# Optimization experiments

Hardware: AMD Instinct MI355X
Metric: run time of the kernel (lower is better)

The kernel has to match this reference:

```python
import jax, jax.numpy as jnp
import numpy as np

B, C, Ci, H, W = 8, 256, 128, 64, 64
EPS = 1e-5


def conv1x1(x, w, b):
    # x: [B,C,H,W], w: [O,C], b: [O] -> [B,O,H,W]
    return jnp.einsum('bchw,oc->bohw', x, w) + b[None, :, None, None]


def maxpool2(x):
    b, c, h, w = x.shape
    return x.reshape(b, c, h // 2, 2, w // 2, 2).max(axis=(3, 5))


def setup_inputs() -> dict:
    key = jax.random.key(0)
    ks = jax.random.split(key, 12)
    s_in = 1.0 / np.sqrt(C)
    s_ic = 1.0 / np.sqrt(Ci)
    return {
        'x': jax.random.normal(ks[0], (B, C, H, W), dtype=jnp.float32),
        'g_w': jax.random.normal(ks[1], (Ci, C), dtype=jnp.float32) * s_in,
        'g_b': jax.random.normal(ks[2], (Ci,), dtype=jnp.float32) * 0.01,
        'theta_w': jax.random.normal(ks[3], (Ci, C), dtype=jnp.float32) * s_in,
        'theta_b': jax.random.normal(ks[4], (Ci,), dtype=jnp.float32) * 0.01,
        'phi_w': jax.random.normal(ks[5], (Ci, C), dtype=jnp.float32) * s_in,
        'phi_b': jax.random.normal(ks[6], (Ci,), dtype=jnp.float32) * 0.01,
        'W_w': jax.random.normal(ks[7], (C, Ci), dtype=jnp.float32) * s_ic,
        'W_b': jax.random.normal(ks[8], (C,), dtype=jnp.float32) * 0.01,
        'bn_gamma': jax.random.normal(ks[9], (C,), dtype=jnp.float32) * 0.1 + 1.0,
        'bn_beta': jax.random.normal(ks[10], (C,), dtype=jnp.float32) * 0.1,
        'bn_mean': jnp.zeros((C,), dtype=jnp.float32),
        'bn_var': jax.random.uniform(ks[11], (C,), dtype=jnp.float32) * 0.5 + 0.75,
    }


def reference(x, g_w, g_b, theta_w, theta_b, phi_w, phi_b, W_w, W_b, bn_gamma, bn_beta, bn_mean, bn_var):
    b = x.shape[0]
    # g and phi: 1x1 conv then 2x2 max-pool (sub_sample=True)
    g_x = maxpool2(conv1x1(x, g_w, g_b)).reshape(b, Ci, -1)          # [B,Ci,Np]
    g_x = jnp.transpose(g_x, (0, 2, 1))                               # [B,Np,Ci]
    theta_x = conv1x1(x, theta_w, theta_b).reshape(b, Ci, -1)         # [B,Ci,N]
    theta_x = jnp.transpose(theta_x, (0, 2, 1))                       # [B,N,Ci]
    phi_x = maxpool2(conv1x1(x, phi_w, phi_b)).reshape(b, Ci, -1)     # [B,Ci,Np]
    f = jnp.einsum('bnc,bcm->bnm', theta_x, phi_x)                    # [B,N,Np]
    f_div_C = jax.nn.softmax(f, axis=-1)                              # embedded_gaussian: plain softmax, no scaling
    y = jnp.einsum('bnm,bmc->bnc', f_div_C, g_x)                      # [B,N,Ci]
    y = jnp.transpose(y, (0, 2, 1)).reshape(b, Ci, H, W)              # [B,Ci,H,W]
    # W: 1x1 conv + BatchNorm (inference form with running stats)
    W_y = conv1x1(y, W_w, W_b)
    inv = bn_gamma / jnp.sqrt(bn_var + EPS)
    W_y = (W_y - bn_mean[None, :, None, None]) * inv[None, :, None, None] + bn_beta[None, :, None, None]
    return W_y + x
```

## Files before the change

### kernel.cpp

```cpp
#include <hip/hip_runtime.h>
#include <math.h>

#define Bn   8
#define Cc   256
#define Cin  128
#define Hh   64
#define Ww   64
#define Nn   4096
#define Npl  1024
#define EPSf 1e-5f

typedef __attribute__((ext_vector_type(8))) short    short8;
typedef __attribute__((ext_vector_type(8))) _Float16 half8;
typedef __attribute__((ext_vector_type(4))) float    floatx4;

__device__ __forceinline__ unsigned short f2bf(float f) {
    unsigned int u = __float_as_uint(f);
    u += 0x7fffu + ((u >> 16) & 1u);
    return (unsigned short)(u >> 16);
}
__device__ __forceinline__ unsigned short f2h(float f) {
    _Float16 h = (_Float16)f;
    return __builtin_bit_cast(unsigned short, h);
}
__device__ __forceinline__ float h2f(unsigned short u) {
    return (float)__builtin_bit_cast(_Float16, u);
}

__device__ __forceinline__ unsigned int cvtpk_bf16(float lo, float hi) {
    unsigned int r;
    asm("v_cvt_pk_bf16_f32 %0, %1, %2" : "=v"(r) : "v"(lo), "v"(hi));
    return r;
}

__device__ __forceinline__ void gload_lds16(const unsigned short* g, unsigned short* l) {
    __builtin_amdgcn_global_load_lds(
        (const __attribute__((address_space(1))) unsigned int*)g,
        (__attribute__((address_space(3))) unsigned int*)l, 16, 0, 0);
}

__global__ __launch_bounds__(256) void k_prep(
    const float* __restrict__ g_w, const float* __restrict__ th_w,
    const float* __restrict__ ph_w,
    const float* __restrict__ W_w, const float* __restrict__ W_b,
    const float* __restrict__ gamma, const float* __restrict__ beta,
    const float* __restrict__ mean,  const float* __restrict__ var,
    unsigned short* __restrict__ gWh,
    unsigned short* __restrict__ thWh, unsigned short* __restrict__ thWl,
    unsigned short* __restrict__ phWh, unsigned short* __restrict__ phWl,
    unsigned short* __restrict__ Wh, float* __restrict__ cvec)
{
    int i = blockIdx.x * 256 + threadIdx.x;
    if (i < 98304) {
        int seg = i >> 15;
        int idx = i & 32767;
        float v = (seg == 0 ? g_w : (seg == 1 ? th_w : ph_w))[idx];
        unsigned short hi = f2h(v);
        if (seg == 0) gWh[idx] = hi;
        else {
            (seg == 1 ? thWh : phWh)[idx] = hi;
            (seg == 1 ? thWl : phWl)[idx] = f2h(v - h2f(hi));
        }
    } else {
        int j = i - 98304;
        int o = j >> 7;
        float inv = gamma[o] * rsqrtf(var[o] + EPSf);
        Wh[j] = f2h(W_w[j] * inv);
        if (j < Cc) {
            float invi = gamma[j] * rsqrtf(var[j] + EPSf);
            cvec[j] = (W_b[j] - mean[j]) * invi + beta[j];
        }
    }
}

#define XPAD 264

__global__ __launch_bounds__(256, 2) void k_conv3(
    const float* __restrict__ x,
    const unsigned short* __restrict__ gWh,
    const unsigned short* __restrict__ thWh, const unsigned short* __restrict__ thWl,
    const unsigned short* __restrict__ phWh, const unsigned short* __restrict__ phWl,
    const float* __restrict__ g_b, const float* __restrict__ th_b,
    const float* __restrict__ ph_b,
    unsigned short* __restrict__ thetaT,
    unsigned short* __restrict__ gPc,
    unsigned short* __restrict__ phiPt)
{
    __shared__ __align__(16) unsigned short Xhi[64 * XPAD];
    __shared__ __align__(16) unsigned short Xlo[64 * XPAD];

    const int t    = threadIdx.x;
    const int w    = t >> 6;
    const int l    = t & 63;
    const int quad = l >> 4;
    const int l16  = l & 15;
    const int b    = blockIdx.x >> 6;
    const int tile = blockIdx.x & 63;
    const int ty   = tile >> 1;
    const int tx   = tile & 1;

    {
        const float4* xg = (const float4*)x;
        unsigned int* XhiW = (unsigned int*)Xhi;
        unsigned int* XloW = (unsigned int*)Xlo;
        #pragma unroll
        for (int it = 0; it < 8; ++it) {
            int idx = t + 256 * it;
            int c2  = idx >> 4;
            int p4  = idx & 15;
            int n   = (2 * ty + (p4 >> 3)) * Ww + tx * 32 + (p4 & 7) * 4;
            float4 va = xg[((size_t)(b * Cc + 2 * c2) * Nn + n) >> 2];
            float4 vb = xg[((size_t)(b * Cc + 2 * c2 + 1) * Nn + n) >> 2];
            const float fa[4] = {va.x, va.y, va.z, va.w};
            const float fb[4] = {vb.x, vb.y, vb.z, vb.w};
            #pragma unroll
            for (int i = 0; i < 4; ++i) {
                int px = p4 * 4 + i;
                unsigned short ha = f2h(fa[i]), hb = f2h(fb[i]);
                unsigned short la = f2h(fa[i] - h2f(ha));
                unsigned short lb = f2h(fb[i] - h2f(hb));
                XhiW[px * 132 + c2] = (unsigned int)ha | ((unsigned int)hb << 16);
                XloW[px * 132 + c2] = (unsigned int)la | ((unsigned int)lb << 16);
            }
        }
    }
    __syncthreads();

    floatx4 acc[6][4] = {};

    #pragma unroll 2
    for (int kd = 0; kd < 8; ++kd) {
        half8 bhi[4], blo[4];
        #pragma unroll
        for (int nt = 0; nt < 4; ++nt) {
            bhi[nt] = *(const half8*)&Xhi[(nt * 16 + l16) * XPAD + kd * 32 + quad * 8];
            blo[nt] = *(const half8*)&Xlo[(nt * 16 + l16) * XPAD + kd * 32 + quad * 8];
        }
        #pragma unroll
        for (int ti = 0; ti < 6; ++ti) {
            int ot  = w + 4 * ti;
            int seg = ot >> 3;
            size_t aoff = (size_t)((ot & 7) * 16 + l16) * Cc + kd * 32 + quad * 8;
            const unsigned short* wh = (seg == 0 ? gWh : (seg == 1 ? thWh : phWh));
            half8 ah = *(const half8*)&wh[aoff];
            #pragma unroll
            for (int nt = 0; nt < 4; ++nt)
                acc[ti][nt] = __builtin_amdgcn_mfma_f32_16x16x32_f16(ah, bhi[nt], acc[ti][nt], 0, 0, 0);
            if (seg != 0) {
                const unsigned short* wl = (seg == 1 ? thWl : phWl);
                half8 al = *(const half8*)&wl[aoff];
                #pragma unroll
                for (int nt = 0; nt < 4; ++nt) {
                    acc[ti][nt] = __builtin_amdgcn_mfma_f32_16x16x32_f16(ah, blo[nt], acc[ti][nt], 0, 0, 0);
                    acc[ti][nt] = __builtin_amdgcn_mfma_f32_16x16x32_f16(al, bhi[nt], acc[ti][nt], 0, 0, 0);
                }
            }
        }
    }

    #pragma unroll
    for (int ti = 0; ti < 6; ++ti) {
        int ot  = w + 4 * ti;
        int seg = ot >> 3;
        int ol  = (ot & 7) * 16 + quad * 4;
        if (seg == 1) {
            float b0 = th_b[ol], b1 = th_b[ol + 1], b2 = th_b[ol + 2], b3 = th_b[ol + 3];
            #pragma unroll
            for (int nt = 0; nt < 4; ++nt) {
                int n = (2 * ty + (nt >> 1)) * Ww + tx * 32 + (nt & 1) * 16 + l16;
                ushort4 v;
                v.x = f2h(acc[ti][nt][0] + b0);
                v.y = f2h(acc[ti][nt][1] + b1);
                v.z = f2h(acc[ti][nt][2] + b2);
                v.w = f2h(acc[ti][nt][3] + b3);
                *(ushort4*)&thetaT[((size_t)b * Nn + n) * Cin + ol] = v;
            }
        } else {
            const float* bb = (seg == 0 ? g_b : ph_b);
            float b0 = bb[ol], b1 = bb[ol + 1], b2 = bb[ol + 2], b3 = bb[ol + 3];
            #pragma unroll
            for (int pp = 0; pp < 2; ++pp) {
                float pm[4];
                #pragma unroll
                for (int r = 0; r < 4; ++r) {
                    float m = fmaxf(acc[ti][pp][r], acc[ti][pp + 2][r]);
                    pm[r] = fmaxf(m, __shfl_xor(m, 1, 64));
                }
                int np = ty * 32 + tx * 16 + pp * 8 + (l16 >> 1);
                if ((l16 & 1) == 0) {
                    if (seg == 0) {
                        gPc[((size_t)b * Cin + ol + 0) * Npl + np] = f2bf(pm[0] + b0);
                        gPc[((size_t)b * Cin + ol + 1) * Npl + np] = f2bf(pm[1] + b1);
                        gPc[((size_t)b * Cin + ol + 2) * Npl + np] = f2bf(pm[2] + b2);
                        gPc[((size_t)b * Cin + ol + 3) * Npl + np] = f2bf(pm[3] + b3);
                    } else {
                        ushort4 v;
                        v.x = f2h(pm[0] + b0); v.y = f2h(pm[1] + b1);
                        v.z = f2h(pm[2] + b2); v.w = f2h(pm[3] + b3);
                        *(ushort4*)&phiPt[((size_t)b * Npl + np) * Cin + ol] = v;
                    }
                }
            }
        }
    }
}

#define SSHIFT 20.0f

__global__ __launch_bounds__(256, 2) void k_attn_out(
    const unsigned short* __restrict__ thetaT,
    const unsigned short* __restrict__ phiPt,
    const unsigned short* __restrict__ gPc,
    const unsigned short* __restrict__ Wh,
    const float* __restrict__ cvec,
    const float* __restrict__ x,
    float* __restrict__ out)
{
    __shared__ __align__(16) unsigned short smem[40960];

    const int t    = threadIdx.x;
    const int w    = t >> 6;
    const int l    = t & 63;
    const int quad = l >> 4;
    const int l16  = l & 15;
    const int bid  = blockIdx.x;
    const int wid  = (bid & 7) * 64 + (bid >> 3);
    const int b    = wid >> 6;
    const int qb   = wid & 63;
    const int n0   = qb * 64;

    uint4 qr[4];
    #pragma unroll
    for (int kd = 0; kd < 4; ++kd)
        qr[kd] = *(const uint4*)&thetaT[((size_t)b * Nn + n0 + w * 16 + l16) * Cin
                                        + kd * 32 + quad * 8];
    #pragma unroll
    for (int kd = 0; kd < 4; ++kd)
        asm volatile("" : "+v"(qr[kd].x), "+v"(qr[kd].y), "+v"(qr[kd].z), "+v"(qr[kd].w));
    half8 qf[4];
    #pragma unroll
    for (int kd = 0; kd < 4; ++kd) qf[kd] = __builtin_bit_cast(half8, qr[kd]);

    floatx4 yacc[8] = {};
    float liq = 0.f;

    const int mK = l >> 4;
    const int gK = l & 15;
    const int cV = l >> 3;
    const int gV = l & 7;

    auto stageKV = [&](int chg, int sel) {
        unsigned short* Ks = smem + sel * 16384;
        unsigned short* Vt = Ks + 8192;
        #pragma unroll
        for (int j = 0; j < 4; ++j) {
            int slot = w * 4 + j;
            int m  = slot * 4 + mK;
            int gs = gK ^ (m & 7);
            gload_lds16(&phiPt[((size_t)b * Npl + chg * 64 + m) * Cin + gs * 8],
                        &Ks[slot * 512]);
        }
        #pragma unroll
        for (int j = 0; j < 4; ++j) {
            int slot = w * 4 + j;
            int c  = slot * 8 + cV;
            int gs = gV ^ (c & 7);
            gload_lds16(&gPc[((size_t)b * Cin + c) * Npl + chg * 64 + gs * 8],
                        &Vt[slot * 512]);
        }
    };

    stageKV(0, 0);
    asm volatile("s_waitcnt vmcnt(0)" ::: "memory");
    __syncthreads();

    #pragma unroll 2
    for (int ch = 0; ch < 16; ++ch) {
        const int cur = ch & 1;
        if (ch < 15) stageKV(ch + 1, cur ^ 1);

        const unsigned short* Ks = smem + cur * 16384;
        const unsigned short* Vt = Ks + 8192;

        floatx4 sacc[4] = {};
        #pragma unroll
        for (int mt = 0; mt < 4; ++mt) {
            #pragma unroll
            for (int kd = 0; kd < 4; ++kd) {
                half8 kf = *(const half8*)&Ks[(mt * 16 + l16) * 128
                                              + (((kd * 4 + quad) ^ (l16 & 7)) << 3)];
                sacc[mt] = __builtin_amdgcn_mfma_f32_16x16x32_f16(kf, qf[kd], sacc[mt], 0, 0, 0);
            }
        }

        float ex[4][4];
        #pragma unroll
        for (int mt = 0; mt < 4; ++mt) {
            #pragma unroll
            for (int r = 0; r < 4; ++r) {
                float v = __expf(sacc[mt][r] - SSHIFT);
                ex[mt][r] = v;
                liq += v;
            }
        }

        short8 pf[2];
        #pragma unroll
        for (int kd = 0; kd < 2; ++kd) {
            unsigned int a0 = cvtpk_bf16(ex[2 * kd][0],     ex[2 * kd][1]);
            unsigned int a1 = cvtpk_bf16(ex[2 * kd + 1][0], ex[2 * kd + 1][1]);
            unsigned int b0 = cvtpk_bf16(ex[2 * kd][2],     ex[2 * kd][3]);
            unsigned int b1 = cvtpk_bf16(ex[2 * kd + 1][2], ex[2 * kd + 1][3]);
            asm volatile("v_permlane32_swap_b32 %0, %1" : "+v"(a0), "+v"(a1));
            asm volatile("v_permlane16_swap_b32 %0, %1" : "+v"(a0), "+v"(a1));
            asm volatile("v_permlane32_swap_b32 %0, %1" : "+v"(b0), "+v"(b1));
            asm volatile("v_permlane16_swap_b32 %0, %1" : "+v"(b0), "+v"(b1));
            uint4 pw; pw.x = a0; pw.y = b0; pw.z = a1; pw.w = b1;
            pf[kd] = __builtin_bit_cast(short8, pw);
        }

        #pragma unroll
        for (int ct = 0; ct < 8; ++ct) {
            #pragma unroll
            for (int kd = 0; kd < 2; ++kd) {
                short8 vf = *(const short8*)&Vt[(ct * 16 + l16) * 64
                                                + (((kd * 4 + quad) ^ (l16 & 7)) << 3)];
                yacc[ct] = __builtin_amdgcn_mfma_f32_16x16x32_bf16(pf[kd], vf, yacc[ct], 0, 0, 0);
            }
        }

        asm volatile("s_waitcnt vmcnt(0)" ::: "memory");
        __syncthreads();
    }

    liq += __shfl_xor(liq, 16, 64);
    liq += __shfl_xor(liq, 32, 64);

    {
        unsigned short* Ws = smem + 8192;
        #pragma unroll
        for (int j = 0; j < 16; ++j) {
            int slot = w * 16 + j;
            int row  = slot * 4 + mK;
            int gs   = gK ^ (row & 7);
            gload_lds16(&Wh[(size_t)row * Cin + gs * 8], &Ws[slot * 512]);
        }
    }

    {
        unsigned short* Ys = smem;
        #pragma unroll
        for (int r = 0; r < 4; ++r) {
            float lr = __shfl(liq, quad * 4 + r, 64);
            float il = 1.0f / lr;
            int q = w * 16 + quad * 4 + r;
            #pragma unroll
            for (int ct = 0; ct < 8; ++ct) {
                int g = ct * 2 + (l16 >> 3);
                Ys[q * 128 + (((g ^ (q & 7)) << 3) | (l16 & 7))] = f2h(yacc[ct][r] * il);
            }
        }
    }
    asm volatile("s_waitcnt vmcnt(0)" ::: "memory");
    __syncthreads();

    const unsigned short* Ys = smem;
    const unsigned short* Ws = smem + 8192;

    #pragma unroll
    for (int oc = 0; oc < 2; ++oc) {
        half8 af[2][4];
        #pragma unroll
        for (int mt = 0; mt < 2; ++mt)
            #pragma unroll
            for (int kd = 0; kd < 4; ++kd) {
                int row = oc * 128 + w * 32 + mt * 16 + l16;
                af[mt][kd] = *(const half8*)&Ws[row * 128
                                                + (((kd * 4 + quad) ^ (l16 & 7)) << 3)];
            }

        floatx4 acc[2][4] = {};
        #pragma unroll
        for (int nt = 0; nt < 4; ++nt) {
            half8 bfr[4];
            #pragma unroll
            for (int kd = 0; kd < 4; ++kd)
                bfr[kd] = *(const half8*)&Ys[(nt * 16 + l16) * 128
                                             + (((kd * 4 + quad) ^ (l16 & 7)) << 3)];
            #pragma unroll
            for (int mt = 0; mt < 2; ++mt)
                #pragma unroll
                for (int kd = 0; kd < 4; ++kd)
                    acc[mt][nt] = __builtin_amdgcn_mfma_f32_16x16x32_f16(af[mt][kd], bfr[kd], acc[mt][nt], 0, 0, 0);
        }

        #pragma unroll
        for (int mt = 0; mt < 2; ++mt) {
            #pragma unroll
            for (int r = 0; r < 4; ++r) {
                int o = oc * 128 + w * 32 + mt * 16 + quad * 4 + r;
                float cv = cvec[o];
                #pragma unroll
                for (int nt = 0; nt < 4; ++nt) {
                    size_t gi = ((size_t)(b * Cc + o)) * Nn + n0 + nt * 16 + l16;
                    out[gi] = acc[mt][nt][r] + cv + x[gi];
                }
            }
        }
    }
}

extern "C" void kernel_launch(void* const* d_in, const int* in_sizes, int n_in,
                              void* d_out, int out_size, void* d_ws, size_t ws_size,
                              hipStream_t stream) {
    const float* x    = (const float*)d_in[0];
    const float* g_w  = (const float*)d_in[1];
    const float* g_b  = (const float*)d_in[2];
    const float* th_w = (const float*)d_in[3];
    const float* th_b = (const float*)d_in[4];
    const float* ph_w = (const float*)d_in[5];
    const float* ph_b = (const float*)d_in[6];
    const float* W_w  = (const float*)d_in[7];
    const float* W_b  = (const float*)d_in[8];
    const float* gmm  = (const float*)d_in[9];
    const float* bta  = (const float*)d_in[10];
    const float* mmn  = (const float*)d_in[11];
    const float* vvr  = (const float*)d_in[12];
    float* out = (float*)d_out;

    unsigned short* thetaT = (unsigned short*)d_ws;
    unsigned short* phiPt  = thetaT + (size_t)4194304;
    unsigned short* gPc    = phiPt + (size_t)1048576;
    unsigned short* Wh     = gPc + (size_t)1048576;
    unsigned short* gWh    = Wh + 32768;
    unsigned short* thWh   = gWh + 32768;
    unsigned short* thWl   = thWh + 32768;
    unsigned short* phWh   = thWl + 32768;
    unsigned short* phWl   = phWh + 32768;
    float*          cvec   = (float*)(phWl + 32768);

    k_prep<<<dim3(512), dim3(256), 0, stream>>>(
        g_w, th_w, ph_w, W_w, W_b, gmm, bta, mmn, vvr,
        gWh, thWh, thWl, phWh, phWl, Wh, cvec);
    k_conv3<<<dim3(Bn * 64), dim3(256), 0, stream>>>(
        x, gWh, thWh, thWl, phWh, phWl, g_b, th_b, ph_b, thetaT, gPc, phiPt);
    k_attn_out<<<dim3(Bn * 64), dim3(256), 0, stream>>>(
        thetaT, phiPt, gPc, Wh, cvec, x, out);
}
```

Baseline: 164.3 us.

## Split attention key chunks across two wave groups with 512-thread blocks

Doubles the attention block to 8 waves. Each pair of waves shares the same query rows and handles half of each 64-key chunk: the loads are split into K and V roles, and partial outputs and row sums are reduced through shared memory at the end. The output projection is also spread across all 8 waves, and the fp16 Y stores are packed into 32-bit writes using lane shuffles. This raises wave-level parallelism per block to hide latency, at the cost of an extra LDS reduction and two more barriers, and it needs the register budget to fit 512 threads.

```diff
diff --git a/kernel.cpp b/kernel.cpp
--- a/kernel.cpp
+++ b/kernel.cpp
@@ -205,9 +205,38 @@
     }
 }
 
+__device__ __forceinline__ void stage_kv(
+    unsigned short* smem, int sel, int chg, int b, int grp, int wq,
+    int mK, int gK, int cV, int gV,
+    const unsigned short* __restrict__ phiPt,
+    const unsigned short* __restrict__ gPc)
+{
+    unsigned short* Kb = smem + sel * 16384;
+    if (grp == 0) {
+        #pragma unroll
+        for (int j = 0; j < 4; ++j) {
+            int slot = wq * 4 + j;
+            int m  = slot * 4 + mK;
+            int gs = gK ^ (m & 7);
+            gload_lds16(&phiPt[((size_t)b * Npl + chg * 64 + m) * Cin + gs * 8],
+                        &Kb[slot * 512]);
+        }
+    } else {
+        unsigned short* Vb = Kb + 8192;
+        #pragma unroll
+        for (int j = 0; j < 4; ++j) {
+            int slot = wq * 4 + j;
+            int c  = slot * 8 + cV;
+            int gs = gV ^ (c & 7);
+            gload_lds16(&gPc[((size_t)b * Cin + c) * Npl + chg * 64 + gs * 8],
+                        &Vb[slot * 512]);
+        }
+    }
+}
+
 #define SSHIFT 20.0f
 
-__global__ __launch_bounds__(256, 2) void k_attn_out(
+__global__ __launch_bounds__(512, 4) void k_attn_out(
     const unsigned short* __restrict__ thetaT,
     const unsigned short* __restrict__ phiPt,
     const unsigned short* __restrict__ gPc,
@@ -220,6 +249,8 @@
 
     const int t    = threadIdx.x;
     const int w    = t >> 6;
+    const int wq   = w & 3;
+    const int grp  = w >> 2;
     const int l    = t & 63;
     const int quad = l >> 4;
     const int l16  = l & 15;
@@ -232,7 +263,7 @@
     uint4 qr[4];
     #pragma unroll
     for (int kd = 0; kd < 4; ++kd)
-        qr[kd] = *(const uint4*)&thetaT[((size_t)b * Nn + n0 + w * 16 + l16) * Cin
+        qr[kd] = *(const uint4*)&thetaT[((size_t)b * Nn + n0 + wq * 16 + l16) * Cin
                                         + kd * 32 + quad * 8];
     #pragma unroll
     for (int kd = 0; kd < 4; ++kd)
@@ -249,84 +280,55 @@
     const int cV = l >> 3;
     const int gV = l & 7;
 
-    auto stageKV = [&](int chg, int sel) {
-        unsigned short* Ks = smem + sel * 16384;
-        unsigned short* Vt = Ks + 8192;
-        #pragma unroll
-        for (int j = 0; j < 4; ++j) {
-            int slot = w * 4 + j;
-            int m  = slot * 4 + mK;
-            int gs = gK ^ (m & 7);
-            gload_lds16(&phiPt[((size_t)b * Npl + chg * 64 + m) * Cin + gs * 8],
-                        &Ks[slot * 512]);
-        }
-        #pragma unroll
-        for (int j = 0; j < 4; ++j) {
-            int slot = w * 4 + j;
-            int c  = slot * 8 + cV;
-            int gs = gV ^ (c & 7);
-            gload_lds16(&gPc[((size_t)b * Cin + c) * Npl + chg * 64 + gs * 8],
-                        &Vt[slot * 512]);
-        }
-    };
-
-    stageKV(0, 0);
+    stage_kv(smem, 0, 0, b, grp, wq, mK, gK, cV, gV, phiPt, gPc);
     asm volatile("s_waitcnt vmcnt(0)" ::: "memory");
     __syncthreads();
 
     #pragma unroll 2
     for (int ch = 0; ch < 16; ++ch) {
         const int cur = ch & 1;
-        if (ch < 15) stageKV(ch + 1, cur ^ 1);
+        if (ch < 15)
+            stage_kv(smem, cur ^ 1, ch + 1, b, grp, wq, mK, gK, cV, gV, phiPt, gPc);
 
         const unsigned short* Ks = smem + cur * 16384;
         const unsigned short* Vt = Ks + 8192;
 
-        floatx4 sacc[4] = {};
-        #pragma unroll
-        for (int mt = 0; mt < 4; ++mt) {
+        floatx4 sacc[2] = {};
+        #pragma unroll
+        for (int mtl = 0; mtl < 2; ++mtl) {
+            int mt = grp * 2 + mtl;
             #pragma unroll
             for (int kd = 0; kd < 4; ++kd) {
                 half8 kf = *(const half8*)&Ks[(mt * 16 + l16) * 128
                                               + (((kd * 4 + quad) ^ (l16 & 7)) << 3)];
-                sacc[mt] = __builtin_amdgcn_mfma_f32_16x16x32_f16(kf, qf[kd], sacc[mt], 0, 0, 0);
-            }
-        }
-
-        float ex[4][4];
-        #pragma unroll
-        for (int mt = 0; mt < 4; ++mt) {
-            #pragma unroll
-            for (int r = 0; r < 4; ++r) {
-                float v = __expf(sacc[mt][r] - SSHIFT);
-                ex[mt][r] = v;
-                liq += v;
-            }
-        }
-
-        short8 pf[2];
-        #pragma unroll
-        for (int kd = 0; kd < 2; ++kd) {
-            unsigned int a0 = cvtpk_bf16(ex[2 * kd][0],     ex[2 * kd][1]);
-            unsigned int a1 = cvtpk_bf16(ex[2 * kd + 1][0], ex[2 * kd + 1][1]);
-            unsigned int b0 = cvtpk_bf16(ex[2 * kd][2],     ex[2 * kd][3]);
-            unsigned int b1 = cvtpk_bf16(ex[2 * kd + 1][2], ex[2 * kd + 1][3]);
-            asm volatile("v_permlane32_swap_b32 %0, %1" : "+v"(a0), "+v"(a1));
-            asm volatile("v_permlane16_swap_b32 %0, %1" : "+v"(a0), "+v"(a1));
-            asm volatile("v_permlane32_swap_b32 %0, %1" : "+v"(b0), "+v"(b1));
-            asm volatile("v_permlane16_swap_b32 %0, %1" : "+v"(b0), "+v"(b1));
-            uint4 pw; pw.x = a0; pw.y = b0; pw.z = a1; pw.w = b1;
-            pf[kd] = __builtin_bit_cast(short8, pw);
-        }
+                sacc[mtl] = __builtin_amdgcn_mfma_f32_16x16x32_f16(kf, qf[kd], sacc[mtl], 0, 0, 0);
+            }
+        }
+
+        float ex0[4], ex1[4];
+        #pragma unroll
+        for (int r = 0; r < 4; ++r) {
+            ex0[r] = __expf(sacc[0][r] - SSHIFT);
+            ex1[r] = __expf(sacc[1][r] - SSHIFT);
+            liq += ex0[r] + ex1[r];
+        }
+
+        unsigned int a0 = cvtpk_bf16(ex0[0], ex0[1]);
+        unsigned int a1 = cvtpk_bf16(ex1[0], ex1[1]);
+        unsigned int b0 = cvtpk_bf16(ex0[2], ex0[3]);
+        unsigned int b1 = cvtpk_bf16(ex1[2], ex1[3]);
+        asm volatile("v_permlane32_swap_b32 %0, %1" : "+v"(a0), "+v"(a1));
+        asm volatile("v_permlane16_swap_b32 %0, %1" : "+v"(a0), "+v"(a1));
+        asm volatile("v_permlane32_swap_b32 %0, %1" : "+v"(b0), "+v"(b1));
+        asm volatile("v_permlane16_swap_b32 %0, %1" : "+v"(b0), "+v"(b1));
+        uint4 pw; pw.x = a0; pw.y = b0; pw.z = a1; pw.w = b1;
+        short8 pf = __builtin_bit_cast(short8, pw);
 
         #pragma unroll
         for (int ct = 0; ct < 8; ++ct) {
-            #pragma unroll
-            for (int kd = 0; kd < 2; ++kd) {
-                short8 vf = *(const short8*)&Vt[(ct * 16 + l16) * 64
-                                                + (((kd * 4 + quad) ^ (l16 & 7)) << 3)];
-                yacc[ct] = __builtin_amdgcn_mfma_f32_16x16x32_bf16(pf[kd], vf, yacc[ct], 0, 0, 0);
-            }
+            short8 vf = *(const short8*)&Vt[(ct * 16 + l16) * 64
+                                            + (((grp * 4 + quad) ^ (l16 & 7)) << 3)];
+            yacc[ct] = __builtin_amdgcn_mfma_f32_16x16x32_bf16(pf, vf, yacc[ct], 0, 0, 0);
         }
 
         asm volatile("s_waitcnt vmcnt(0)" ::: "memory");
@@ -336,28 +338,52 @@
     liq += __shfl_xor(liq, 16, 64);
     liq += __shfl_xor(liq, 32, 64);
 
+    float* cbuf = (float*)smem;
+    const int ci = (wq * 64 + l) * 33;
+    if (grp == 1) {
+        #pragma unroll
+        for (int ct = 0; ct < 8; ++ct)
+            #pragma unroll
+            for (int r = 0; r < 4; ++r) cbuf[ci + ct * 4 + r] = yacc[ct][r];
+        cbuf[ci + 32] = liq;
+    }
+    __syncthreads();
+    if (grp == 0) {
+        #pragma unroll
+        for (int ct = 0; ct < 8; ++ct)
+            #pragma unroll
+            for (int r = 0; r < 4; ++r) yacc[ct][r] += cbuf[ci + ct * 4 + r];
+        liq += cbuf[ci + 32];
+    }
+    __syncthreads();
+
     {
         unsigned short* Ws = smem + 8192;
         #pragma unroll
-        for (int j = 0; j < 16; ++j) {
-            int slot = w * 16 + j;
+        for (int j = 0; j < 8; ++j) {
+            int slot = w * 8 + j;
             int row  = slot * 4 + mK;
             int gs   = gK ^ (row & 7);
             gload_lds16(&Wh[(size_t)row * Cin + gs * 8], &Ws[slot * 512]);
         }
     }
 
-    {
-        unsigned short* Ys = smem;
+    if (grp == 0) {
+        unsigned int* Yw = (unsigned int*)smem;
         #pragma unroll
         for (int r = 0; r < 4; ++r) {
             float lr = __shfl(liq, quad * 4 + r, 64);
             float il = 1.0f / lr;
-            int q = w * 16 + quad * 4 + r;
+            int q  = wq * 16 + quad * 4 + r;
+            int q7 = q & 7;
             #pragma unroll
             for (int ct = 0; ct < 8; ++ct) {
-                int g = ct * 2 + (l16 >> 3);
-                Ys[q * 128 + (((g ^ (q & 7)) << 3) | (l16 & 7))] = f2h(yacc[ct][r] * il);
+                unsigned int h = f2h(yacc[ct][r] * il);
+                unsigned int p = (unsigned int)__shfl_xor((int)h, 1, 64);
+                if ((l16 & 1) == 0) {
+                    int g = ct * 2 + (l16 >> 3);
+                    Yw[q * 64 + (((g ^ q7) << 2) | ((l16 & 7) >> 1))] = h | (p << 16);
+                }
             }
         }
     }
@@ -367,44 +393,41 @@
     const unsigned short* Ys = smem;
     const unsigned short* Ws = smem + 8192;
 
-    #pragma unroll
-    for (int oc = 0; oc < 2; ++oc) {
-        half8 af[2][4];
+    half8 af[2][4];
+    #pragma unroll
+    for (int mt = 0; mt < 2; ++mt)
+        #pragma unroll
+        for (int kd = 0; kd < 4; ++kd) {
+            int row = w * 32 + mt * 16 + l16;
+            af[mt][kd] = *(const half8*)&Ws[row * 128
+                                            + (((kd * 4 + quad) ^ (l16 & 7)) << 3)];
+        }
+
+    floatx4 acc[2][4] = {};
+    #pragma unroll
+    for (int nt = 0; nt < 4; ++nt) {
+        half8 bfr[4];
+        #pragma unroll
+        for (int kd = 0; kd < 4; ++kd)
+            bfr[kd] = *(const half8*)&Ys[(nt * 16 + l16) * 128
+                                         + (((kd * 4 + quad) ^ (l16 & 7)) << 3)];
         #pragma unroll
         for (int mt = 0; mt < 2; ++mt)
             #pragma unroll
-            for (int kd = 0; kd < 4; ++kd) {
-                int row = oc * 128 + w * 32 + mt * 16 + l16;
-                af[mt][kd] = *(const half8*)&Ws[row * 128
-                                                + (((kd * 4 + quad) ^ (l16 & 7)) << 3)];
-            }
-
-        floatx4 acc[2][4] = {};
-        #pragma unroll
-        for (int nt = 0; nt < 4; ++nt) {
-            half8 bfr[4];
-            #pragma unroll
             for (int kd = 0; kd < 4; ++kd)
-                bfr[kd] = *(const half8*)&Ys[(nt * 16 + l16) * 128
-                                             + (((kd * 4 + quad) ^ (l16 & 7)) << 3)];
-            #pragma unroll
-            for (int mt = 0; mt < 2; ++mt)
-                #pragma unroll
-                for (int kd = 0; kd < 4; ++kd)
-                    acc[mt][nt] = __builtin_amdgcn_mfma_f32_16x16x32_f16(af[mt][kd], bfr[kd], acc[mt][nt], 0, 0, 0);
-        }
-
-        #pragma unroll
-        for (int mt = 0; mt < 2; ++mt) {
-            #pragma unroll
-            for (int r = 0; r < 4; ++r) {
-                int o = oc * 128 + w * 32 + mt * 16 + quad * 4 + r;
-                float cv = cvec[o];
-                #pragma unroll
-                for (int nt = 0; nt < 4; ++nt) {
-                    size_t gi = ((size_t)(b * Cc + o)) * Nn + n0 + nt * 16 + l16;
-                    out[gi] = acc[mt][nt][r] + cv + x[gi];
-                }
+                acc[mt][nt] = __builtin_amdgcn_mfma_f32_16x16x32_f16(af[mt][kd], bfr[kd], acc[mt][nt], 0, 0, 0);
+    }
+
+    #pragma unroll
+    for (int mt = 0; mt < 2; ++mt) {
+        #pragma unroll
+        for (int r = 0; r < 4; ++r) {
+            int o = w * 32 + mt * 16 + quad * 4 + r;
+            float cv = cvec[o];
+            #pragma unroll
+            for (int nt = 0; nt < 4; ++nt) {
+                size_t gi = ((size_t)(b * Cc + o)) * Nn + n0 + nt * 16 + l16;
+                out[gi] = acc[mt][nt][r] + cv + x[gi];
             }
         }
     }
@@ -444,6 +467,6 @@
         gWh, thWh, thWl, phWh, phWl, Wh, cvec);
     k_conv3<<<dim3(Bn * 64), dim3(256), 0, stream>>>(
         x, gWh, thWh, thWl, phWh, phWl, g_b, th_b, ph_b, thetaT, gPc, phiPt);
-    k_attn_out<<<dim3(Bn * 64), dim3(256), 0, stream>>>(
+    k_attn_out<<<dim3(Bn * 64), dim3(512), 0, stream>>>(
         thetaT, phiPt, gPc, Wh, cvec, x, out);
 }
```

New measurement: 165.7 us. Within noise of the previous version (+0.8%).
